# Kernel tuning notes

Hardware: AMD Instinct MI355X
Metric: run time of the kernel (lower is better)

The kernel has to match this reference:

```python
import jax, jax.numpy as jnp
import numpy as np

B_SZ, L, H, D, N, R, K = 2, 1024, 2048, 4096, 16, 128, 4


def setup_inputs() -> dict:
    key = jax.random.key(0)
    ks = jax.random.split(key, 10)
    s = lambda *sh: 1.0 / np.sqrt(sh[-1])
    inp = {
        "hidden_states": jax.random.normal(ks[0], (B_SZ, L, H), jnp.float32),
        "in_proj_w": jax.random.normal(ks[1], (2 * D, H), jnp.float32) * s(H),
        "conv_w": jax.random.normal(ks[2], (D, 1, K), jnp.float32) * s(K),
        "conv_b": jax.random.normal(ks[3], (D,), jnp.float32) * 0.02,
        "x_proj_w": jax.random.normal(ks[4], (R + 2 * N, D), jnp.float32) * s(D),
        "dt_proj_w": jax.random.normal(ks[5], (D, R), jnp.float32) * s(R),
        "dt_proj_b": jax.random.normal(ks[6], (D,), jnp.float32) * 0.02,
        # A_log = log(arange(1, N+1)) broadcast over D, as in the module init
        "A_log": jnp.broadcast_to(jnp.log(jnp.arange(1, N + 1, dtype=jnp.float32))[None, :], (D, N)),
        "D_param": jnp.ones((D,), jnp.float32),
        "out_proj_w": jax.random.normal(ks[7], (H, D), jnp.float32) * s(D),
    }
    return inp


def _mamba_forward(hidden_states, in_proj_w, conv_w, conv_b, x_proj_w,
                   dt_proj_w, dt_proj_b, A_log, D_param, out_proj_w):
    silu = jax.nn.silu
    # in_proj: [B,L,H] @ [H,2D] -> [B,L,2D] -> [B,2D,L]
    proj = jnp.einsum("blh,ph->bpl", hidden_states, in_proj_w)
    u, gate = jnp.split(proj, 2, axis=1)  # each [B,D,L]
    # depthwise causal conv1d (padding K-1 on the left, then first L outputs)
    u = jax.lax.conv_general_dilated(
        u, conv_w, window_strides=(1,), padding=[(K - 1, 0)],
        dimension_numbers=("NCH", "OIH", "NCH"), feature_group_count=D,
    ) + conv_b[None, :, None]
    u = silu(u)  # [B,D,L]
    # x_proj on [B,L,D]
    ssm_params = jnp.einsum("bdl,pd->blp", u, x_proj_w)  # [B,L,R+2N]
    time_step, Bmat, Cmat = jnp.split(ssm_params, [R, R + N], axis=-1)
    # dt_proj + softplus -> [B,D,L]
    dt = jnp.einsum("blr,dr->bld", time_step, dt_proj_w) + dt_proj_b
    dt = jax.nn.softplus(dt).transpose(0, 2, 1)  # [B,D,L]
    A = -jnp.exp(A_log)  # [D,N]

    # selective scan over time; carry ssm_state [B,D,N]
    def step(state, xs):
        dt_t, B_t, C_t, u_t = xs  # [B,D],[B,N],[B,N],[B,D]
        dA = jnp.exp(A[None] * dt_t[:, :, None])          # [B,D,N]
        dBu = dt_t[:, :, None] * B_t[:, None, :] * u_t[:, :, None]
        state = dA * state + dBu
        y_t = jnp.einsum("bdn,bn->bd", state, C_t)        # [B,D]
        return state, y_t

    xs = (dt.transpose(2, 0, 1),          # [L,B,D]
          Bmat.transpose(1, 0, 2),        # [L,B,N]
          Cmat.transpose(1, 0, 2),        # [L,B,N]
          u.transpose(2, 0, 1))           # [L,B,D]
    init = jnp.zeros((hidden_states.shape[0], D, N), hidden_states.dtype)
    _, ys = jax.lax.scan(step, init, xs)   # ys [L,B,D]
    y = ys.transpose(1, 2, 0)              # [B,D,L]
    y = y + u * D_param[None, :, None]
    y = y * silu(gate)
    # out_proj: [B,L,D] @ [D,H]
    return jnp.einsum("bdl,hd->blh", y, out_proj_w)


def reference(hidden_states, in_proj_w, conv_w, conv_b, x_proj_w,
              dt_proj_w, dt_proj_b, A_log, D_param, out_proj_w):
    return _mamba_forward(hidden_states, in_proj_w, conv_w, conv_b, x_proj_w,
                          dt_proj_w, dt_proj_b, A_log, D_param, out_proj_w)
```

## Files before the change

### kernel.cpp

```cpp
#include <hip/hip_runtime.h>

#define L_SEQ 1024
#define DD 4096
#define NC 32
#define CT 32

typedef short bf16x8 __attribute__((ext_vector_type(8)));
typedef float f32x4 __attribute__((ext_vector_type(4)));
typedef unsigned short u16;

typedef const __attribute__((address_space(1))) void gas_t;
typedef __attribute__((address_space(3))) void las_t;

__device__ inline u16 f2bf(float f) {
  unsigned int u = __float_as_uint(f);
  u = (u + 0x7FFFu + ((u >> 16) & 1u)) >> 16;
  return (u16)u;
}

__device__ inline float bf2f(u16 v) {
  return __uint_as_float(((unsigned int)v) << 16);
}

__device__ inline float softplusf(float x) {
  return x > 20.f ? x : log1pf(expf(x));
}

__global__ __launch_bounds__(256) void cast_all_k(
    const float* __restrict__ hs, const float* __restrict__ w_in,
    const float* __restrict__ xw, const float* __restrict__ dtw,
    const float* __restrict__ ow, u16* __restrict__ hs_bf,
    u16* __restrict__ win_bf, u16* __restrict__ xw_bf,
    u16* __restrict__ dtw_bf, u16* __restrict__ ow_bf) {
  const int blk = blockIdx.x;
  const float* s;
  u16* d;
  int base;
  if (blk < 4096)        { s = hs;   d = hs_bf;  base = blk; }
  else if (blk < 20480)  { s = w_in; d = win_bf; base = blk - 4096; }
  else if (blk < 21120)  { s = xw;   d = xw_bf;  base = blk - 20480; }
  else if (blk < 21632)  { s = dtw;  d = dtw_bf; base = blk - 21120; }
  else                   { s = ow;   d = ow_bf;  base = blk - 21632; }
  const int i = (base * 256 + threadIdx.x) * 4;
  float4 v = *(const float4*)(s + i);
  ushort4 o;
  o.x = f2bf(v.x); o.y = f2bf(v.y); o.z = f2bf(v.z); o.w = f2bf(v.w);
  *(ushort4*)(d + i) = o;
}

__global__ __launch_bounds__(256) void reduce4_k(const float* __restrict__ p,
                                                 float* __restrict__ out,
                                                 long n) {
  long i = ((long)blockIdx.x * 256 + threadIdx.x) * 4;
  if (i >= n) return;
  float4 a = *(const float4*)(p + i);
  float4 b = *(const float4*)(p + n + i);
  float4 c = *(const float4*)(p + 2 * n + i);
  float4 d = *(const float4*)(p + 3 * n + i);
  float4 o;
  o.x = (a.x + b.x) + (c.x + d.x);
  o.y = (a.y + b.y) + (c.y + d.y);
  o.z = (a.z + b.z) + (c.z + d.z);
  o.w = (a.w + b.w) + (c.w + d.w);
  *(float4*)(out + i) = o;
}

__global__ __launch_bounds__(256) void xproj_fin_k(const float* __restrict__ parts,
                                                   u16* __restrict__ ts,
                                                   float* __restrict__ ssm) {
  const int idx = blockIdx.x * 256 + threadIdx.x;
  float s = 0.f;
#pragma unroll
  for (int z = 0; z < 8; z++) s += parts[z * 327680 + idx];
  const int row = idx / 160;
  const int col = idx - row * 160;
  if (col < 128) ts[row * 128 + col] = f2bf(s);
  else ssm[idx] = s;
}

template <int CMODE, bool SWZ>
__global__ __launch_bounds__(512, 2) void gemm256(const u16* __restrict__ A,
                                                  const u16* __restrict__ B,
                                                  void* __restrict__ Cv,
                                                  int Nld, int K, int kc,
                                                  long zstride) {
  __shared__ u16 lds[2][2][8192];
  const int tid = threadIdx.x;
  const int lane = tid & 63, wid = tid >> 6;
  const int wm = wid >> 2, wn = wid & 3;
  int ty = blockIdx.y, tx = blockIdx.x;
  if (SWZ) {
    int flat = blockIdx.y * 32 + blockIdx.x;
    int xcd = flat & 7, pos = flat >> 3;
    ty = (xcd & 1) * 4 + (pos >> 3);
    tx = (xcd >> 1) * 8 + (pos & 7);
  }
  const long tm = (long)ty * 256, tn = (long)tx * 256;

  const int ksw = ((lane >> 4) ^ (lane & 3) ^ ((lane >> 2) & 3)) * 8;

  const long ks0 = (CMODE == 2) ? (long)blockIdx.z * kc : 0;

  const int srow = tid >> 2;
  const u16* gA0 = A + (tm + srow) * (long)K + ks0 + ksw;
  const u16* gA1 = A + (tm + 128 + srow) * (long)K + ks0 + ksw;
  const u16* gB0 = B + (tn + srow) * (long)K + ks0 + ksw;
  const u16* gB1 = B + (tn + 128 + srow) * (long)K + ks0 + ksw;
  const int sb0 = wid * 512;
  const int sb1 = 4096 + wid * 512;

  f32x4 acc[8][4] = {};

  const int lr = lane & 15;
  const int arow = wm * 128 + lr;
  const int brow = wn * 64 + lr;

  const int KT = kc >> 5;

#define STG(buf, kt)                                                           \
  {                                                                            \
    const long ko_ = (long)(kt) << 5;                                          \
    __builtin_amdgcn_global_load_lds((gas_t*)(gA0 + ko_),                      \
                                     (las_t*)&lds[buf][0][sb0], 16, 0, 0);     \
    __builtin_amdgcn_global_load_lds((gas_t*)(gA1 + ko_),                      \
                                     (las_t*)&lds[buf][0][sb1], 16, 0, 0);     \
    __builtin_amdgcn_global_load_lds((gas_t*)(gB0 + ko_),                      \
                                     (las_t*)&lds[buf][1][sb0], 16, 0, 0);     \
    __builtin_amdgcn_global_load_lds((gas_t*)(gB1 + ko_),                      \
                                     (las_t*)&lds[buf][1][sb1], 16, 0, 0);     \
  }

  STG(0, 0);
  if (KT > 1) STG(1, 1);

  for (int kt = 0; kt < KT; ++kt) {
    const int c = kt & 1;
    if (kt + 1 < KT)
      asm volatile("s_waitcnt vmcnt(4)" ::: "memory");
    else
      asm volatile("s_waitcnt vmcnt(0)" ::: "memory");
    __builtin_amdgcn_sched_barrier(0);
    __builtin_amdgcn_s_barrier();
    bf16x8 af[8], bfr[4];
#pragma unroll
    for (int n = 0; n < 4; n++)
      bfr[n] = *(const bf16x8*)&lds[c][1][(brow + n * 16) * 32 + ksw];
#pragma unroll
    for (int m = 0; m < 8; m++)
      af[m] = *(const bf16x8*)&lds[c][0][(arow + m * 16) * 32 + ksw];
    __builtin_amdgcn_s_setprio(1);
#pragma unroll
    for (int m = 0; m < 8; m++)
#pragma unroll
      for (int n = 0; n < 4; n++)
        acc[m][n] = __builtin_amdgcn_mfma_f32_16x16x32_bf16(af[m], bfr[n],
                                                            acc[m][n], 0, 0, 0);
    __builtin_amdgcn_s_setprio(0);
    __builtin_amdgcn_sched_barrier(0);
    __builtin_amdgcn_s_barrier();
    __builtin_amdgcn_sched_barrier(0);
    if (kt + 2 < KT) STG(c, kt + 2);
  }
#undef STG

  float* Cf = (CMODE == 2) ? (float*)Cv + (long)blockIdx.z * zstride
                           : (float*)Cv;

  const int rg = (lane >> 4) * 4;
#pragma unroll
  for (int m = 0; m < 8; m++) {
    const long gr = tm + wm * 128 + m * 16 + rg;
#pragma unroll
    for (int n = 0; n < 4; n++) {
      const long gc = tn + wn * 64 + n * 16 + lr;
#pragma unroll
      for (int r = 0; r < 4; r++) {
        if (CMODE == 1)
          ((u16*)Cv)[(gr + r) * (long)Nld + gc] = f2bf(acc[m][n][r]);
        else
          Cf[(gr + r) * (long)Nld + gc] = acc[m][n][r];
      }
    }
  }
}

template <bool CLAMP_N, int MODE>
__global__ __launch_bounds__(256) void gemm_bt(const u16* __restrict__ A,
                                               const u16* __restrict__ B,
                                               void* __restrict__ Cv,
                                               const float* __restrict__ ebias,
                                               int Nv, int K, int ldc, int kc,
                                               long zs) {
  __shared__ u16 lA[128 * 32];
  __shared__ u16 lB[128 * 32];
  const int tid = threadIdx.x;
  const int lane = tid & 63, wid = tid >> 6;
  const int wm = wid >> 1, wn = wid & 1;
  const long tm = (long)blockIdx.y * 128, tn = (long)blockIdx.x * 128;

  f32x4 acc[4][4] = {};

  const int rowoff = lane >> 2;
  const int ko = (lane & 3) * 8;
  const int c0 = wid * 2, c1 = c0 + 1;
  const long ra0 = tm + c0 * 16 + rowoff;
  const long ra1 = tm + c1 * 16 + rowoff;
  long rb0 = tn + c0 * 16 + rowoff;
  long rb1 = tn + c1 * 16 + rowoff;
  if (CLAMP_N) {
    if (rb0 >= Nv) rb0 = Nv - 1;
    if (rb1 >= Nv) rb1 = Nv - 1;
  }
  const u16* gA0 = A + ra0 * K + ko;
  const u16* gA1 = A + ra1 * K + ko;
  const u16* gB0 = B + rb0 * K + ko;
  const u16* gB1 = B + rb1 * K + ko;
  u16* sA0 = &lA[c0 * 512];
  u16* sA1 = &lA[c1 * 512];
  u16* sB0 = &lB[c0 * 512];
  u16* sB1 = &lB[c1 * 512];

  int ks0 = 0, ks1 = K;
  if (MODE == 2) { ks0 = blockIdx.z * kc; ks1 = ks0 + kc; }

  const int lr = lane & 15, kq = (lane >> 4) * 8;
  const int arow = wm * 64 + lr, brow = wn * 64 + lr;

  for (int ks = ks0; ks < ks1; ks += 32) {
    __builtin_amdgcn_global_load_lds((gas_t*)(gA0 + ks), (las_t*)sA0, 16, 0, 0);
    __builtin_amdgcn_global_load_lds((gas_t*)(gA1 + ks), (las_t*)sA1, 16, 0, 0);
    __builtin_amdgcn_global_load_lds((gas_t*)(gB0 + ks), (las_t*)sB0, 16, 0, 0);
    __builtin_amdgcn_global_load_lds((gas_t*)(gB1 + ks), (las_t*)sB1, 16, 0, 0);
    __syncthreads();
    bf16x8 af[4], bfr[4];
#pragma unroll
    for (int i = 0; i < 4; i++) {
      af[i]  = *(const bf16x8*)&lA[(arow + i * 16) * 32 + kq];
      bfr[i] = *(const bf16x8*)&lB[(brow + i * 16) * 32 + kq];
    }
#pragma unroll
    for (int i = 0; i < 4; i++)
#pragma unroll
      for (int j = 0; j < 4; j++)
        acc[i][j] = __builtin_amdgcn_mfma_f32_16x16x32_bf16(af[i], bfr[j],
                                                            acc[i][j], 0, 0, 0);
    __syncthreads();
  }

  float* Cf = (MODE == 2) ? (float*)Cv + (long)blockIdx.z * zs : (float*)Cv;

  const int rg = (lane >> 4) * 4;
#pragma unroll
  for (int i = 0; i < 4; i++) {
    const long gr = tm + wm * 64 + i * 16 + rg;
#pragma unroll
    for (int j = 0; j < 4; j++) {
      const long gc = tn + wn * 64 + j * 16 + lr;
      if (CLAMP_N && gc >= Nv) continue;
      float bias = 0.f;
      if (MODE == 1) bias = ebias[gc];
#pragma unroll
      for (int r = 0; r < 4; r++) {
        float v = acc[i][j][r];
        if (MODE == 1)
          ((u16*)Cv)[(gr + r) * (long)ldc + gc] = f2bf(softplusf(v + bias));
        else
          Cf[(gr + r) * (long)ldc + gc] = v;
      }
    }
  }
}

__global__ __launch_bounds__(256) void conv_silu_k(const u16* __restrict__ projb,
                                                   const float* __restrict__ cw,
                                                   const float* __restrict__ cb,
                                                   u16* __restrict__ ub) {
  const int idx = blockIdx.x * 256 + threadIdx.x;
  const int d = idx & (DD - 1);
  const int bl = idx >> 12;
  const int l = bl & (L_SEQ - 1);
  const float4 w = *(const float4*)(cw + d * 4);
  float s = cb[d];
  const u16* pp = projb + (long)bl * 8192 + d;
  s += w.w * bf2f(pp[0]);
  if (l >= 1) s += w.z * bf2f(pp[-8192]);
  if (l >= 2) s += w.y * bf2f(pp[-2 * 8192]);
  if (l >= 3) s += w.x * bf2f(pp[-3 * 8192]);
  const float r = s / (1.f + expf(-s));
  ub[idx] = f2bf(r);
}

__global__ __launch_bounds__(256) void scan_p1(const u16* __restrict__ dt,
                                               const u16* __restrict__ u,
                                               const float* __restrict__ ssm,
                                               const float* __restrict__ A_log,
                                               float* __restrict__ Sbuf,
                                               float* __restrict__ Pbuf) {
  __shared__ float sBC[CT * 32];
  const int tid = threadIdx.x;
  const int d = blockIdx.x * 256 + tid;
  const int c = blockIdx.y, b = blockIdx.z;
  const long blbase = (long)b * L_SEQ + (long)c * CT;
  for (int i = tid; i < CT * 32; i += 256) {
    int tt = i >> 5, j = i & 31;
    sBC[i] = ssm[(blbase + tt) * 160 + 128 + j];
  }
  __syncthreads();
  float a2[16], st[16], pr[16];
#pragma unroll
  for (int g = 0; g < 4; g++) {
    float4 al = *(const float4*)(A_log + d * 16 + g * 4);
    a2[g*4+0] = -expf(al.x) * 1.4426950408889634f;
    a2[g*4+1] = -expf(al.y) * 1.4426950408889634f;
    a2[g*4+2] = -expf(al.z) * 1.4426950408889634f;
    a2[g*4+3] = -expf(al.w) * 1.4426950408889634f;
  }
#pragma unroll
  for (int n = 0; n < 16; n++) { st[n] = 0.f; pr[n] = 1.f; }
  for (int tt = 0; tt < CT; tt++) {
    const long bl = blbase + tt;
    const float dtv = bf2f(dt[bl * DD + d]);
    const float uv = bf2f(u[bl * DD + d]);
    const float dtu = dtv * uv;
    const float4* Bv = (const float4*)&sBC[tt * 32];
#pragma unroll
    for (int g = 0; g < 4; g++) {
      const float4 Bg = Bv[g];
      float e;
      e = exp2f(a2[g*4+0]*dtv); st[g*4+0] = e*st[g*4+0] + dtu*Bg.x; pr[g*4+0] *= e;
      e = exp2f(a2[g*4+1]*dtv); st[g*4+1] = e*st[g*4+1] + dtu*Bg.y; pr[g*4+1] *= e;
      e = exp2f(a2[g*4+2]*dtv); st[g*4+2] = e*st[g*4+2] + dtu*Bg.z; pr[g*4+2] *= e;
      e = exp2f(a2[g*4+3]*dtv); st[g*4+3] = e*st[g*4+3] + dtu*Bg.w; pr[g*4+3] *= e;
    }
  }
  const long base = (((long)b * NC + c) * DD + d) * 16;
#pragma unroll
  for (int g = 0; g < 4; g++) {
    *(float4*)(Sbuf + base + g * 4) = make_float4(st[g*4+0], st[g*4+1], st[g*4+2], st[g*4+3]);
    *(float4*)(Pbuf + base + g * 4) = make_float4(pr[g*4+0], pr[g*4+1], pr[g*4+2], pr[g*4+3]);
  }
}

__global__ __launch_bounds__(256) void scan_p2(const float* __restrict__ Sbuf,
                                               const float* __restrict__ Pbuf,
                                               float* __restrict__ carry) {
  const int idx = blockIdx.x * 256 + threadIdx.x;
  const int ng = idx & 3;
  const int d = (idx >> 2) & (DD - 1);
  const int b = idx >> 14;
  float4 cr = make_float4(0.f, 0.f, 0.f, 0.f);
  for (int c = 0; c < NC; c++) {
    const long base = (((long)b * NC + c) * DD + d) * 16 + ng * 4;
    *(float4*)(carry + base) = cr;
    const float4 P = *(const float4*)(Pbuf + base);
    const float4 S = *(const float4*)(Sbuf + base);
    cr.x = P.x * cr.x + S.x;
    cr.y = P.y * cr.y + S.y;
    cr.z = P.z * cr.z + S.z;
    cr.w = P.w * cr.w + S.w;
  }
}

__global__ __launch_bounds__(256) void scan_p3(const u16* __restrict__ dt,
                                               const u16* __restrict__ u,
                                               const float* __restrict__ ssm,
                                               const u16* __restrict__ projb,
                                               const float* __restrict__ A_log,
                                               const float* __restrict__ Dp,
                                               const float* __restrict__ carry,
                                               u16* __restrict__ yb) {
  __shared__ float sBC[CT * 32];
  const int tid = threadIdx.x;
  const int d = blockIdx.x * 256 + tid;
  const int c = blockIdx.y, b = blockIdx.z;
  const long blbase = (long)b * L_SEQ + (long)c * CT;
  for (int i = tid; i < CT * 32; i += 256) {
    int tt = i >> 5, j = i & 31;
    sBC[i] = ssm[(blbase + tt) * 160 + 128 + j];
  }
  __syncthreads();
  float a2[16], st[16];
#pragma unroll
  for (int g = 0; g < 4; g++) {
    float4 al = *(const float4*)(A_log + d * 16 + g * 4);
    a2[g*4+0] = -expf(al.x) * 1.4426950408889634f;
    a2[g*4+1] = -expf(al.y) * 1.4426950408889634f;
    a2[g*4+2] = -expf(al.z) * 1.4426950408889634f;
    a2[g*4+3] = -expf(al.w) * 1.4426950408889634f;
  }
  const long cbase = (((long)b * NC + c) * DD + d) * 16;
#pragma unroll
  for (int g = 0; g < 4; g++) {
    float4 cv = *(const float4*)(carry + cbase + g * 4);
    st[g*4+0] = cv.x; st[g*4+1] = cv.y; st[g*4+2] = cv.z; st[g*4+3] = cv.w;
  }
  const float dp = Dp[d];
  for (int tt = 0; tt < CT; tt++) {
    const long bl = blbase + tt;
    const float dtv = bf2f(dt[bl * DD + d]);
    const float uv = bf2f(u[bl * DD + d]);
    const float dtu = dtv * uv;
    float acc = 0.f;
    const float4* Bv = (const float4*)&sBC[tt * 32];
    const float4* Cv = Bv + 4;
#pragma unroll
    for (int g = 0; g < 4; g++) {
      const float4 Bg = Bv[g];
      const float4 Cg = Cv[g];
      float e;
      e = exp2f(a2[g*4+0]*dtv); st[g*4+0] = e*st[g*4+0] + dtu*Bg.x; acc += st[g*4+0]*Cg.x;
      e = exp2f(a2[g*4+1]*dtv); st[g*4+1] = e*st[g*4+1] + dtu*Bg.y; acc += st[g*4+1]*Cg.y;
      e = exp2f(a2[g*4+2]*dtv); st[g*4+2] = e*st[g*4+2] + dtu*Bg.z; acc += st[g*4+2]*Cg.z;
      e = exp2f(a2[g*4+3]*dtv); st[g*4+3] = e*st[g*4+3] + dtu*Bg.w; acc += st[g*4+3]*Cg.w;
    }
    const float g = bf2f(projb[bl * 8192 + DD + d]);
    const float yv = (acc + uv * dp) * (g / (1.f + expf(-g)));
    yb[bl * DD + d] = f2bf(yv);
  }
}

extern "C" void kernel_launch(void* const* d_in, const int* in_sizes, int n_in,
                              void* d_out, int out_size, void* d_ws, size_t ws_size,
                              hipStream_t stream) {
  const float* hs     = (const float*)d_in[0];
  const float* w_in   = (const float*)d_in[1];
  const float* conv_w = (const float*)d_in[2];
  const float* conv_b = (const float*)d_in[3];
  const float* xw     = (const float*)d_in[4];
  const float* dtw    = (const float*)d_in[5];
  const float* dtb    = (const float*)d_in[6];
  const float* A_log  = (const float*)d_in[7];
  const float* Dp     = (const float*)d_in[8];
  const float* ow     = (const float*)d_in[9];
  float* out = (float*)d_out;

  constexpr size_t SZ_HS_BF  = 2048ull * 2048 * 2;
  constexpr size_t SZ_WIN_BF = 8192ull * 2048 * 2;
  constexpr size_t SZ_PROJ   = 2048ull * 8192 * 2;
  constexpr size_t SZ_UBF    = 2048ull * 4096 * 2;
  constexpr size_t SZ_XW_BF  = 160ull * 4096 * 2;
  constexpr size_t SZ_SSM    = 2048ull * 160 * 4;
  constexpr size_t SZ_TS_BF  = 2048ull * 128 * 2;
  constexpr size_t SZ_DTW_BF = 4096ull * 128 * 2;
  constexpr size_t SZ_DT     = 2048ull * 4096 * 2;
  constexpr size_t SZ_OW_BF  = 2048ull * 4096 * 2;
  constexpr size_t SZ_YBF    = 2048ull * 4096 * 2;
  constexpr size_t SZ_SCAN   = 2ull * NC * DD * 16 * 4;
  constexpr size_t SZ_PXP    = 8ull * 2048 * 160 * 4;
  constexpr size_t TOTAL = SZ_HS_BF + SZ_WIN_BF + SZ_PROJ + SZ_UBF +
                           SZ_XW_BF + SZ_SSM + SZ_TS_BF + SZ_DTW_BF + SZ_DT +
                           SZ_OW_BF + SZ_YBF + 3 * SZ_SCAN + SZ_PXP;
  if (ws_size < TOTAL) return;

  char* w = (char*)d_ws;
  u16* hs_bf   = (u16*)w;   w += SZ_HS_BF;
  u16* win_bf  = (u16*)w;   w += SZ_WIN_BF;
  u16* projb   = (u16*)w;   w += SZ_PROJ;
  u16* u_bf    = (u16*)w;   w += SZ_UBF;
  u16* xw_bf   = (u16*)w;   w += SZ_XW_BF;
  float* ssm   = (float*)w; w += SZ_SSM;
  u16* ts_bf   = (u16*)w;   w += SZ_TS_BF;
  u16* dtw_bf  = (u16*)w;   w += SZ_DTW_BF;
  u16* dt_bf   = (u16*)w;   w += SZ_DT;
  u16* ow_bf   = (u16*)w;   w += SZ_OW_BF;
  u16* y_bf    = (u16*)w;   w += SZ_YBF;
  float* Sbuf  = (float*)w; w += SZ_SCAN;
  float* Pbuf  = (float*)w; w += SZ_SCAN;
  float* carry = (float*)w; w += SZ_SCAN;
  float* partsx = (float*)w; w += SZ_PXP;

  float* parts = (float*)win_bf;

  cast_all_k<<<29824, 256, 0, stream>>>(hs, w_in, xw, dtw, ow,
                                        hs_bf, win_bf, xw_bf, dtw_bf, ow_bf);

  gemm256<1, true><<<dim3(32, 8), 512, 0, stream>>>(
      hs_bf, win_bf, projb, 8192, 2048, 2048, 0);

  conv_silu_k<<<32768, 256, 0, stream>>>(projb, conv_w, conv_b, u_bf);

  gemm_bt<true, 2><<<dim3(2, 16, 8), 256, 0, stream>>>(
      u_bf, xw_bf, partsx, nullptr, 160, 4096, 160, 512, 327680);

  xproj_fin_k<<<1280, 256, 0, stream>>>(partsx, ts_bf, ssm);

  gemm_bt<false, 1><<<dim3(32, 16), 256, 0, stream>>>(
      ts_bf, dtw_bf, dt_bf, dtb, 4096, 128, 4096, 0, 0);

  scan_p1<<<dim3(16, NC, 2), 256, 0, stream>>>(dt_bf, u_bf, ssm, A_log, Sbuf, Pbuf);
  scan_p2<<<128, 256, 0, stream>>>(Sbuf, Pbuf, carry);
  scan_p3<<<dim3(16, NC, 2), 256, 0, stream>>>(dt_bf, u_bf, ssm, projb, A_log, Dp,
                                               carry, y_bf);

  gemm256<2, false><<<dim3(8, 8, 4), 512, 0, stream>>>(
      y_bf, ow_bf, parts, 2048, 4096, 1024, 2048ll * 2048);
  reduce4_k<<<4096, 256, 0, stream>>>(parts, out, 2048ll * 2048);
}
```

Baseline: 366.8 us.

## Rework GEMM pipeline to prefetch-one-ahead, change LDS swizzle, and retune scan chunking

```diff
diff --git a/kernel.cpp b/kernel.cpp
--- a/kernel.cpp
+++ b/kernel.cpp
@@ -2,8 +2,8 @@
 
 #define L_SEQ 1024
 #define DD 4096
-#define NC 32
-#define CT 32
+#define NC 16
+#define CT 64
 
 typedef short bf16x8 __attribute__((ext_vector_type(8)));
 typedef float f32x4 __attribute__((ext_vector_type(4)));
@@ -97,71 +97,58 @@
   }
   const long tm = (long)ty * 256, tn = (long)tx * 256;
 
-  const int ksw = ((lane >> 4) ^ (lane & 3) ^ ((lane >> 2) & 3)) * 8;
-
   const long ks0 = (CMODE == 2) ? (long)blockIdx.z * kc : 0;
 
   const int srow = tid >> 2;
-  const u16* gA0 = A + (tm + srow) * (long)K + ks0 + ksw;
-  const u16* gA1 = A + (tm + 128 + srow) * (long)K + ks0 + ksw;
-  const u16* gB0 = B + (tn + srow) * (long)K + ks0 + ksw;
-  const u16* gB1 = B + (tn + 128 + srow) * (long)K + ks0 + ksw;
+  const int sks = (((tid & 3) ^ ((srow >> 1) & 3))) * 8;
+  const u16* gA0 = A + (tm + srow) * (long)K + ks0 + sks;
+  const u16* gA1 = A + (tm + 128 + srow) * (long)K + ks0 + sks;
+  const u16* gB0 = B + (tn + srow) * (long)K + ks0 + sks;
+  const u16* gB1 = B + (tn + 128 + srow) * (long)K + ks0 + sks;
   const int sb0 = wid * 512;
   const int sb1 = 4096 + wid * 512;
 
   f32x4 acc[8][4] = {};
 
-  const int lr = lane & 15;
+  const int lr = lane & 15, kq = lane >> 4;
   const int arow = wm * 128 + lr;
   const int brow = wn * 64 + lr;
+  const int granA = (kq ^ ((arow >> 1) & 3)) * 8;
+  const int granB = (kq ^ ((brow >> 1) & 3)) * 8;
 
   const int KT = kc >> 5;
-
-#define STG(buf, kt)                                                           \
-  {                                                                            \
-    const long ko_ = (long)(kt) << 5;                                          \
-    __builtin_amdgcn_global_load_lds((gas_t*)(gA0 + ko_),                      \
-                                     (las_t*)&lds[buf][0][sb0], 16, 0, 0);     \
-    __builtin_amdgcn_global_load_lds((gas_t*)(gA1 + ko_),                      \
-                                     (las_t*)&lds[buf][0][sb1], 16, 0, 0);     \
-    __builtin_amdgcn_global_load_lds((gas_t*)(gB0 + ko_),                      \
-                                     (las_t*)&lds[buf][1][sb0], 16, 0, 0);     \
-    __builtin_amdgcn_global_load_lds((gas_t*)(gB1 + ko_),                      \
-                                     (las_t*)&lds[buf][1][sb1], 16, 0, 0);     \
-  }
-
-  STG(0, 0);
-  if (KT > 1) STG(1, 1);
+  int cur = 0;
+  __builtin_amdgcn_global_load_lds((gas_t*)gA0, (las_t*)&lds[0][0][sb0], 16, 0, 0);
+  __builtin_amdgcn_global_load_lds((gas_t*)gA1, (las_t*)&lds[0][0][sb1], 16, 0, 0);
+  __builtin_amdgcn_global_load_lds((gas_t*)gB0, (las_t*)&lds[0][1][sb0], 16, 0, 0);
+  __builtin_amdgcn_global_load_lds((gas_t*)gB1, (las_t*)&lds[0][1][sb1], 16, 0, 0);
+  __syncthreads();
 
   for (int kt = 0; kt < KT; ++kt) {
-    const int c = kt & 1;
-    if (kt + 1 < KT)
-      asm volatile("s_waitcnt vmcnt(4)" ::: "memory");
-    else
-      asm volatile("s_waitcnt vmcnt(0)" ::: "memory");
-    __builtin_amdgcn_sched_barrier(0);
-    __builtin_amdgcn_s_barrier();
+    if (kt + 1 < KT) {
+      const long ko = (long)(kt + 1) << 5;
+      const int nb = cur ^ 1;
+      __builtin_amdgcn_global_load_lds((gas_t*)(gA0 + ko), (las_t*)&lds[nb][0][sb0], 16, 0, 0);
+      __builtin_amdgcn_global_load_lds((gas_t*)(gA1 + ko), (las_t*)&lds[nb][0][sb1], 16, 0, 0);
+      __builtin_amdgcn_global_load_lds((gas_t*)(gB0 + ko), (las_t*)&lds[nb][1][sb0], 16, 0, 0);
+      __builtin_amdgcn_global_load_lds((gas_t*)(gB1 + ko), (las_t*)&lds[nb][1][sb1], 16, 0, 0);
+    }
     bf16x8 af[8], bfr[4];
 #pragma unroll
     for (int n = 0; n < 4; n++)
-      bfr[n] = *(const bf16x8*)&lds[c][1][(brow + n * 16) * 32 + ksw];
+      bfr[n] = *(const bf16x8*)&lds[cur][1][(brow + n * 16) * 32 + granB];
 #pragma unroll
     for (int m = 0; m < 8; m++)
-      af[m] = *(const bf16x8*)&lds[c][0][(arow + m * 16) * 32 + ksw];
-    __builtin_amdgcn_s_setprio(1);
+      af[m] = *(const bf16x8*)&lds[cur][0][(arow + m * 16) * 32 + granA];
 #pragma unroll
     for (int m = 0; m < 8; m++)
 #pragma unroll
       for (int n = 0; n < 4; n++)
         acc[m][n] = __builtin_amdgcn_mfma_f32_16x16x32_bf16(af[m], bfr[n],
                                                             acc[m][n], 0, 0, 0);
-    __builtin_amdgcn_s_setprio(0);
-    __builtin_amdgcn_sched_barrier(0);
-    __builtin_amdgcn_s_barrier();
-    __builtin_amdgcn_sched_barrier(0);
-    if (kt + 2 < KT) STG(c, kt + 2);
-  }
-#undef STG
+    __syncthreads();
+    cur ^= 1;
+  }
 
   float* Cf = (CMODE == 2) ? (float*)Cv + (long)blockIdx.z * zstride
                            : (float*)Cv;
@@ -200,21 +187,21 @@
 
   f32x4 acc[4][4] = {};
 
-  const int rowoff = lane >> 2;
-  const int ko = (lane & 3) * 8;
+  const int roff = lane >> 2;
+  const int sks = (((lane & 3) ^ ((roff >> 1) & 3))) * 8;
   const int c0 = wid * 2, c1 = c0 + 1;
-  const long ra0 = tm + c0 * 16 + rowoff;
-  const long ra1 = tm + c1 * 16 + rowoff;
-  long rb0 = tn + c0 * 16 + rowoff;
-  long rb1 = tn + c1 * 16 + rowoff;
+  const long ra0 = tm + c0 * 16 + roff;
+  const long ra1 = tm + c1 * 16 + roff;
+  long rb0 = tn + c0 * 16 + roff;
+  long rb1 = tn + c1 * 16 + roff;
   if (CLAMP_N) {
     if (rb0 >= Nv) rb0 = Nv - 1;
     if (rb1 >= Nv) rb1 = Nv - 1;
   }
-  const u16* gA0 = A + ra0 * K + ko;
-  const u16* gA1 = A + ra1 * K + ko;
-  const u16* gB0 = B + rb0 * K + ko;
-  const u16* gB1 = B + rb1 * K + ko;
+  const u16* gA0 = A + ra0 * K + sks;
+  const u16* gA1 = A + ra1 * K + sks;
+  const u16* gB0 = B + rb0 * K + sks;
+  const u16* gB1 = B + rb1 * K + sks;
   u16* sA0 = &lA[c0 * 512];
   u16* sA1 = &lA[c1 * 512];
   u16* sB0 = &lB[c0 * 512];
@@ -223,8 +210,10 @@
   int ks0 = 0, ks1 = K;
   if (MODE == 2) { ks0 = blockIdx.z * kc; ks1 = ks0 + kc; }
 
-  const int lr = lane & 15, kq = (lane >> 4) * 8;
+  const int lr = lane & 15, kq = lane >> 4;
   const int arow = wm * 64 + lr, brow = wn * 64 + lr;
+  const int granA = (kq ^ ((arow >> 1) & 3)) * 8;
+  const int granB = (kq ^ ((brow >> 1) & 3)) * 8;
 
   for (int ks = ks0; ks < ks1; ks += 32) {
     __builtin_amdgcn_global_load_lds((gas_t*)(gA0 + ks), (las_t*)sA0, 16, 0, 0);
@@ -235,8 +224,8 @@
     bf16x8 af[4], bfr[4];
 #pragma unroll
     for (int i = 0; i < 4; i++) {
-      af[i]  = *(const bf16x8*)&lA[(arow + i * 16) * 32 + kq];
-      bfr[i] = *(const bf16x8*)&lB[(brow + i * 16) * 32 + kq];
+      af[i]  = *(const bf16x8*)&lA[(arow + i * 16) * 32 + granA];
+      bfr[i] = *(const bf16x8*)&lB[(brow + i * 16) * 32 + granB];
     }
 #pragma unroll
     for (int i = 0; i < 4; i++)
```

Result: slower. 381.1 us (+3.9%).
